# Kernel optimization log

Measured on AMD Instinct MI355X. Metric: run time of the kernel, lower is better.

The kernel has to match this reference:

```python
import jax, jax.numpy as jnp
import numpy as np

B, CIN, COUT, H, W = 8, 128, 256, 64, 64
EPS = 1e-5


def conv2d(x, w, b, pad):
    y = jax.lax.conv_general_dilated(
        x, w, window_strides=(1, 1), padding=[(pad, pad), (pad, pad)],
        dimension_numbers=('NCHW', 'OIHW', 'NCHW'))
    return y + b[None, :, None, None]


def deform_sample(x, offset):
    # x: [B,C,H,W], offset: [B,18,H,W] -> sampled: [B,C,9,H,W]
    b, c, h, w = x.shape
    off = offset.reshape(b, 9, 2, h, w)  # (dy, dx) per kernel tap (torchvision v1 order)
    ky = (jnp.arange(9) // 3 - 1).astype(x.dtype)
    kx = (jnp.arange(9) % 3 - 1).astype(x.dtype)
    py = jnp.arange(h, dtype=x.dtype)[None, None, :, None] + ky[None, :, None, None] + off[:, :, 0]
    px = jnp.arange(w, dtype=x.dtype)[None, None, None, :] + kx[None, :, None, None] + off[:, :, 1]
    y0 = jnp.floor(py); x0 = jnp.floor(px)
    fy = py - y0;       fx = px - x0
    xf = x.reshape(b, c, h * w)

    def gather(iy, ix):
        valid = (iy >= 0) & (iy < h) & (ix >= 0) & (ix < w)
        iyc = jnp.clip(iy, 0, h - 1).astype(jnp.int32)
        ixc = jnp.clip(ix, 0, w - 1).astype(jnp.int32)
        idx = (iyc * w + ixc).reshape(b, -1)  # [B, 9*H*W]
        g = jax.vmap(lambda xb, ib: jnp.take(xb, ib, axis=1))(xf, idx)  # [B,C,9HW]
        return g.reshape(b, c, 9, h, w) * valid.astype(x.dtype)[:, None]

    samp = (gather(y0,     x0    ) * ((1 - fy) * (1 - fx))[:, None]
          + gather(y0,     x0 + 1) * ((1 - fy) * fx      )[:, None]
          + gather(y0 + 1, x0    ) * (fy * (1 - fx)      )[:, None]
          + gather(y0 + 1, x0 + 1) * (fy * fx            )[:, None])
    return samp


def setup_inputs():
    key = jax.random.key(0)
    ks = jax.random.split(key, 8)
    return {
        'x':     jax.random.normal(ks[0], (B, CIN, H, W), jnp.float32),
        'w_off': jax.random.normal(ks[1], (18, CIN, 3, 3), jnp.float32) * 0.01,
        'b_off': jnp.zeros((18,), jnp.float32),
        'w_def': jax.random.normal(ks[2], (COUT, CIN, 3, 3), jnp.float32) * 0.03,
        'b_def': jax.random.normal(ks[3], (COUT,), jnp.float32) * 0.01,
        'gamma': jnp.ones((COUT,), jnp.float32),
        'beta':  jnp.zeros((COUT,), jnp.float32),
        'w_sc':  jax.random.normal(ks[4], (COUT, CIN, 1, 1), jnp.float32) * 0.05,
        'b_sc':  jnp.zeros((COUT,), jnp.float32),
    }


def reference(x, w_off, b_off, w_def, b_def, gamma, beta, w_sc, b_sc):
    offset = conv2d(x, w_off, b_off, pad=1)                 # [B,18,H,W]
    samp = deform_sample(x, offset)                         # [B,C,9,H,W]
    out = jnp.einsum('bckhw,ock->bohw', samp, w_def.reshape(COUT, CIN, 9))
    out = out + b_def[None, :, None, None]
    # BatchNorm2d (training mode: batch statistics)
    mean = out.mean(axis=(0, 2, 3))
    var = out.var(axis=(0, 2, 3))
    out = (out - mean[None, :, None, None]) * jax.lax.rsqrt(var + EPS)[None, :, None, None]
    out = out * gamma[None, :, None, None] + beta[None, :, None, None]
    out = out + conv2d(x, w_sc, b_sc, pad=0)                # residual shortcut (1x1)
    return jax.nn.relu(out)
```

## Files before the change

### kernel.cpp

```cpp
#include <hip/hip_runtime.h>

typedef __attribute__((ext_vector_type(8))) short bf16x8;
typedef __attribute__((ext_vector_type(4))) float f32x4;

__device__ __forceinline__ float bf2f(unsigned short u) {
  return __uint_as_float(((unsigned int)u) << 16);
}
__device__ __forceinline__ unsigned short f2bf(float f) {
  unsigned int u = __float_as_uint(f);
  u += 0x7fffu + ((u >> 16) & 1u);
  return (unsigned short)(u >> 16);
}

constexpr size_t OFF_XPAD = 0;
constexpr size_t SZ_XPAD  = (size_t)8 * 66 * 66 * 128 * 2;
constexpr size_t OFF_WB   = OFF_XPAD + SZ_XPAD;
constexpr size_t SZ_WB    = (size_t)9 * 16 * 256 * 8 * 2;
constexpr size_t OFF_WS2  = OFF_WB + SZ_WB;
constexpr size_t SZ_WS2   = (size_t)16 * 256 * 8 * 2;
constexpr size_t OFF_WO   = OFF_WS2 + SZ_WS2;
constexpr size_t SZ_WO    = (size_t)9 * 16 * 32 * 8 * 2;
constexpr size_t OFF_YM   = OFF_WO + SZ_WO;
constexpr size_t SZ_YM    = (size_t)32768 * 256 * 2;
constexpr size_t OFF_PART = OFF_YM + SZ_YM;
constexpr size_t SZ_PART  = (size_t)512 * 256 * 2 * 4;
constexpr size_t OFF_STAT = OFF_PART + SZ_PART;

__global__ __launch_bounds__(256) void k_prep_x(const float* __restrict__ x,
                                                unsigned short* __restrict__ xp) {
  int blk = blockIdx.x;
  int b = blk >> 6, h = blk & 63;
  int t = threadIdx.x;
  __shared__ float tile[16][66];
  for (int cc = 0; cc < 8; ++cc) {
    int c0 = cc * 16;
    int wr = t & 63, cl = t >> 6;
#pragma unroll
    for (int i = 0; i < 4; ++i) {
      int c = c0 + cl * 4 + i;
      tile[cl * 4 + i][wr] = x[(((size_t)b * 128 + c) * 64 + h) * 64 + wr];
    }
    __syncthreads();
    int ww = t >> 2, cq = t & 3;
    ushort4 u4;
    u4.x = f2bf(tile[cq * 4 + 0][ww]);
    u4.y = f2bf(tile[cq * 4 + 1][ww]);
    u4.z = f2bf(tile[cq * 4 + 2][ww]);
    u4.w = f2bf(tile[cq * 4 + 3][ww]);
    *(ushort4*)(xp + ((size_t)(b * 66 + h + 1) * 66 + (ww + 1)) * 128 + c0 + cq * 4) = u4;
    __syncthreads();
  }
}

__global__ __launch_bounds__(256) void k_pack_w(const float* __restrict__ wdef,
                                                const float* __restrict__ wsc,
                                                const float* __restrict__ woff,
                                                unsigned short* __restrict__ wB,
                                                unsigned short* __restrict__ wS,
                                                unsigned short* __restrict__ wO) {
  int tid = blockIdx.x * 256 + threadIdx.x;
  if (tid < 294912) {
    int k8 = tid & 7, n = (tid >> 3) & 255, kb = (tid >> 11) & 15, tap = tid >> 15;
    int c = kb * 8 + k8;
    wB[tid] = f2bf(wdef[((size_t)n * 128 + c) * 9 + tap]);
  } else if (tid < 294912 + 32768) {
    int i = tid - 294912;
    int k8 = i & 7, n = (i >> 3) & 255, kb = i >> 11;
    wS[i] = f2bf(wsc[(size_t)n * 128 + kb * 8 + k8]);
  } else if (tid < 294912 + 32768 + 36864) {
    int i = tid - 327680;
    int k8 = i & 7, n = (i >> 3) & 31, kb = (i >> 8) & 15, tap = i >> 12;
    int c = kb * 8 + k8;
    wO[i] = f2bf(n < 18 ? woff[((size_t)n * 128 + c) * 9 + tap] : 0.f);
  }
}

__global__ __launch_bounds__(256) void k_main(const unsigned short* __restrict__ xp,
                                              const unsigned short* __restrict__ wB,
                                              const unsigned short* __restrict__ wO,
                                              const float* __restrict__ boff,
                                              const float* __restrict__ bdef,
                                              unsigned short* __restrict__ ymain,
                                              float* __restrict__ partials) {
  int blk = blockIdx.x;
  int b = blk >> 6, h = blk & 63;
  int t = threadIdx.x;
  int lane = t & 63, wid = t >> 6;
  int m = lane & 15, quad = lane >> 4;
  __shared__ __align__(16) unsigned short At[2][64 * 136];
  __shared__ float offsL[9][64][2];

  {
    f32x4 a0 = {0.f, 0.f, 0.f, 0.f}, a1 = {0.f, 0.f, 0.f, 0.f};
    int px = wid * 16 + m;
    const unsigned short* xbase = xp + ((size_t)(b * 66 + h) * 66 + px) * 128 + quad * 8;
    for (int tap = 0; tap < 9; ++tap) {
      const unsigned short* arow = xbase + ((tap / 3) * 66 + (tap % 3)) * 128;
#pragma unroll
      for (int kk = 0; kk < 4; ++kk) {
        bf16x8 a = *(const bf16x8*)(arow + kk * 32);
        const unsigned short* bb = wO + (size_t)(tap * 16 + kk * 4 + quad) * 256;
        bf16x8 b0 = *(const bf16x8*)(bb + m * 8);
        bf16x8 b1 = *(const bf16x8*)(bb + (16 + m) * 8);
        a0 = __builtin_amdgcn_mfma_f32_16x16x32_bf16(a, b0, a0, 0, 0, 0);
        a1 = __builtin_amdgcn_mfma_f32_16x16x32_bf16(a, b1, a1, 0, 0, 0);
      }
    }
#pragma unroll
    for (int r = 0; r < 4; ++r) {
      int pxs = wid * 16 + quad * 4 + r;
      offsL[m >> 1][pxs][m & 1] = a0[r] + boff[m];
      if (m < 2) offsL[8][pxs][m] = a1[r] + boff[16 + m];
    }
  }
  __syncthreads();

  f32x4 acc[4][4];
#pragma unroll
  for (int i = 0; i < 4; ++i)
#pragma unroll
    for (int j = 0; j < 4; ++j) acc[i][j] = (f32x4){0.f, 0.f, 0.f, 0.f};

  int px_s = t >> 2, sub = t & 3;
  const unsigned short* xb_base = xp + (size_t)b * 66 * 66 * 128;
  int nb = wid * 64;

  auto sample_prep = [&](int tap, float* wgt, const unsigned short** p) {
    float2 ov = *(const float2*)&offsL[tap][px_s][0];
    int ky = tap / 3 - 1, kx = tap % 3 - 1;
    float py = (float)(h + ky) + ov.x;
    float pxf = (float)(px_s + kx) + ov.y;
    float y0f = floorf(py), x0f = floorf(pxf);
    float fy = py - y0f, fx = pxf - x0f;
    int iy0 = (int)y0f, ix0 = (int)x0f;
#pragma unroll
    for (int j = 0; j < 4; ++j) {
      int iy = iy0 + (j >> 1), ix = ix0 + (j & 1);
      float wy = (j >> 1) ? fy : 1.f - fy;
      float wx = (j & 1) ? fx : 1.f - fx;
      bool valid = (iy >= 0) && (iy < 64) && (ix >= 0) && (ix < 64);
      int iyc = min(max(iy, 0), 63), ixc = min(max(ix, 0), 63);
      wgt[j] = valid ? wy * wx : 0.f;
      p[j] = xb_base + ((size_t)(iyc + 1) * 66 + (ixc + 1)) * 128 + sub * 8;
    }
  };
  auto load_g2 = [&](const unsigned short** p, int g0, bf16x8 (*v)[4]) {
#pragma unroll
    for (int gg = 0; gg < 2; ++gg)
#pragma unroll
      for (int j = 0; j < 4; ++j)
        v[gg][j] = *(const bf16x8*)(p[j] + (g0 + gg) * 32);
  };
  auto store_g2 = [&](unsigned short* dst, int g0, const float* wgt, bf16x8 (*v)[4]) {
#pragma unroll
    for (int gg = 0; gg < 2; ++gg) {
      bf16x8 o;
#pragma unroll
      for (int j = 0; j < 8; ++j) {
        float s = fmaf(wgt[0], bf2f((unsigned short)v[gg][0][j]),
                  fmaf(wgt[1], bf2f((unsigned short)v[gg][1][j]),
                  fmaf(wgt[2], bf2f((unsigned short)v[gg][2][j]),
                       wgt[3] * bf2f((unsigned short)v[gg][3][j]))));
        o[j] = (short)f2bf(s);
      }
      *(bf16x8*)(dst + (g0 + gg) * 32) = o;
    }
  };
  auto mfma_half = [&](const unsigned short* buf, int tap, int kk0) {
#pragma unroll
    for (int kk = kk0; kk < kk0 + 2; ++kk) {
      bf16x8 af[4];
#pragma unroll
      for (int ms = 0; ms < 4; ++ms)
        af[ms] = *(const bf16x8*)(buf + (ms * 16 + m) * 136 + kk * 32 + quad * 8);
#pragma unroll
      for (int ns = 0; ns < 4; ++ns) {
        bf16x8 bfr = *(const bf16x8*)(wB + ((size_t)(tap * 16 + kk * 4 + quad) * 256 + nb + ns * 16 + m) * 8);
#pragma unroll
        for (int ms = 0; ms < 4; ++ms)
          acc[ms][ns] = __builtin_amdgcn_mfma_f32_16x16x32_bf16(af[ms], bfr, acc[ms][ns], 0, 0, 0);
      }
    }
  };

  {
    float wgt[4]; const unsigned short* p[4]; bf16x8 v[2][4];
    sample_prep(0, wgt, p);
    unsigned short* dst = &At[0][px_s * 136 + sub * 8];
    load_g2(p, 0, v); store_g2(dst, 0, wgt, v);
    load_g2(p, 2, v); store_g2(dst, 2, wgt, v);
  }
#pragma unroll
  for (int tap = 0; tap < 9; ++tap) {
    __syncthreads();
    const unsigned short* cur = At[tap & 1];
    unsigned short* dst = &At[(tap + 1) & 1][px_s * 136 + sub * 8];
    if (tap < 8) {
      float wgt[4]; const unsigned short* p[4]; bf16x8 v[2][4];
      sample_prep(tap + 1, wgt, p);
      load_g2(p, 0, v);
      mfma_half(cur, tap, 0);
      store_g2(dst, 0, wgt, v);
      load_g2(p, 2, v);
      mfma_half(cur, tap, 2);
      store_g2(dst, 2, wgt, v);
    } else {
      mfma_half(cur, tap, 0);
      mfma_half(cur, tap, 2);
    }
  }

  __syncthreads();
  unsigned short* yb = &At[0][0];
#pragma unroll
  for (int ns = 0; ns < 4; ++ns) {
    int n = nb + ns * 16 + m;
    float bias = bdef[n];
    float s = 0.f, q = 0.f;
#pragma unroll
    for (int ms = 0; ms < 4; ++ms) {
#pragma unroll
      for (int r = 0; r < 4; ++r) {
        int px = ms * 16 + quad * 4 + r;
        float v = acc[ms][ns][r] + bias;
        yb[px * 264 + n] = f2bf(v);
        s += v;
        q += v * v;
      }
    }
    s += __shfl_xor(s, 16); s += __shfl_xor(s, 32);
    q += __shfl_xor(q, 16); q += __shfl_xor(q, 32);
    if (quad == 0) {
      partials[((size_t)blk * 256 + n) * 2 + 0] = s;
      partials[((size_t)blk * 256 + n) * 2 + 1] = q;
    }
  }
  __syncthreads();
  {
    unsigned short* grow = ymain + (size_t)(blk * 64 + px_s) * 256;
    const unsigned short* lrow = yb + px_s * 264;
#pragma unroll
    for (int k = 0; k < 8; ++k) {
      int n0 = k * 32 + sub * 8;
      *(bf16x8*)(grow + n0) = *(const bf16x8*)(lrow + n0);
    }
  }
}

__global__ __launch_bounds__(64) void k_stats(const float* __restrict__ partials,
                                              const float* __restrict__ gamma,
                                              const float* __restrict__ beta,
                                              float* __restrict__ stats) {
  int ch = blockIdx.x;
  int L = threadIdx.x;
  float s = 0.f, q = 0.f;
#pragma unroll
  for (int i = 0; i < 8; ++i) {
    int row = i * 64 + L;
    s += partials[((size_t)row * 256 + ch) * 2 + 0];
    q += partials[((size_t)row * 256 + ch) * 2 + 1];
  }
#pragma unroll
  for (int d = 1; d < 64; d <<= 1) { s += __shfl_xor(s, d); q += __shfl_xor(q, d); }
  if (L == 0) {
    float mean = s * (1.f / 32768.f);
    float var = q * (1.f / 32768.f) - mean * mean;
    float inv = rsqrtf(var + 1e-5f);
    float A = gamma[ch] * inv;
    stats[ch * 2 + 0] = A;
    stats[ch * 2 + 1] = beta[ch] - mean * A;
  }
}

__global__ __launch_bounds__(256) void k_final(const unsigned short* __restrict__ xp,
                                               const unsigned short* __restrict__ wS,
                                               const unsigned short* __restrict__ ymain,
                                               const float* __restrict__ stats,
                                               const float* __restrict__ bsc,
                                               float* __restrict__ out) {
  int blk = blockIdx.x;
  int b = blk >> 6, h = blk & 63;
  int t = threadIdx.x;
  int lane = t & 63, wid = t >> 6;
  int m = lane & 15, quad = lane >> 4;
  __shared__ float tr[128 * 67];
  f32x4 acc[4][4];
#pragma unroll
  for (int i = 0; i < 4; ++i)
#pragma unroll
    for (int j = 0; j < 4; ++j) acc[i][j] = (f32x4){0.f, 0.f, 0.f, 0.f};
  const unsigned short* xrow = xp + ((size_t)(b * 66 + h + 1) * 66 + 1) * 128;
  int nb = wid * 64;
#pragma unroll
  for (int kk = 0; kk < 4; ++kk) {
    bf16x8 af[4];
#pragma unroll
    for (int ms = 0; ms < 4; ++ms)
      af[ms] = *(const bf16x8*)(xrow + (ms * 16 + m) * 128 + kk * 32 + quad * 8);
#pragma unroll
    for (int ns = 0; ns < 4; ++ns) {
      bf16x8 bfr = *(const bf16x8*)(wS + ((size_t)(kk * 4 + quad) * 256 + nb + ns * 16 + m) * 8);
#pragma unroll
      for (int ms = 0; ms < 4; ++ms)
        acc[ms][ns] = __builtin_amdgcn_mfma_f32_16x16x32_bf16(af[ms], bfr, acc[ms][ns], 0, 0, 0);
    }
  }
  for (int pass = 0; pass < 2; ++pass) {
    if ((wid >> 1) == pass) {
#pragma unroll
      for (int ns = 0; ns < 4; ++ns) {
        int n = nb + ns * 16 + m;
        float bs = bsc[n];
        int nl = n - pass * 128;
#pragma unroll
        for (int ms = 0; ms < 4; ++ms)
#pragma unroll
          for (int r = 0; r < 4; ++r) {
            int px = ms * 16 + quad * 4 + r;
            tr[nl * 67 + px] = acc[ms][ns][r] + bs;
          }
      }
    }
    __syncthreads();
    {
      int nl = t & 127, g = t >> 7;
      int n = pass * 128 + nl;
      float A = stats[n * 2], Bc = stats[n * 2 + 1];
#pragma unroll 8
      for (int i = 0; i < 32; ++i) {
        int px = g * 32 + i;
        float ym = bf2f(ymain[(size_t)(blk * 64 + px) * 256 + n]);
        float* pt = &tr[nl * 67 + px];
        *pt = fmaxf(fmaf(ym, A, Bc) + *pt, 0.f);
      }
    }
    __syncthreads();
    {
      int ww = t & 63, ng = t >> 6;
#pragma unroll 8
      for (int i = 0; i < 32; ++i) {
        int nl = ng * 32 + i;
        out[((size_t)(b * 256 + pass * 128 + nl) * 64 + h) * 64 + ww] = tr[nl * 67 + ww];
      }
    }
    __syncthreads();
  }
}

extern "C" void kernel_launch(void* const* d_in, const int* in_sizes, int n_in,
                              void* d_out, int out_size, void* d_ws, size_t ws_size,
                              hipStream_t stream) {
  const float* x     = (const float*)d_in[0];
  const float* w_off = (const float*)d_in[1];
  const float* b_off = (const float*)d_in[2];
  const float* w_def = (const float*)d_in[3];
  const float* b_def = (const float*)d_in[4];
  const float* gamma = (const float*)d_in[5];
  const float* beta  = (const float*)d_in[6];
  const float* w_sc  = (const float*)d_in[7];
  const float* b_sc  = (const float*)d_in[8];
  float* out = (float*)d_out;

  char* ws = (char*)d_ws;
  unsigned short* xpad  = (unsigned short*)(ws + OFF_XPAD);
  unsigned short* wB    = (unsigned short*)(ws + OFF_WB);
  unsigned short* wS    = (unsigned short*)(ws + OFF_WS2);
  unsigned short* wO    = (unsigned short*)(ws + OFF_WO);
  unsigned short* ymain = (unsigned short*)(ws + OFF_YM);
  float* partials       = (float*)(ws + OFF_PART);
  float* stats          = (float*)(ws + OFF_STAT);

  hipMemsetAsync(xpad, 0, SZ_XPAD, stream);
  k_prep_x<<<512, 256, 0, stream>>>(x, xpad);
  k_pack_w<<<1424, 256, 0, stream>>>(w_def, w_sc, w_off, wB, wS, wO);
  k_main<<<512, 256, 0, stream>>>(xpad, wB, wO, b_off, b_def, ymain, partials);
  k_stats<<<256, 64, 0, stream>>>(partials, gamma, beta, stats);
  k_final<<<512, 256, 0, stream>>>(xpad, wS, ymain, stats, b_sc, out);
}
```

Before: 162.1 us.

## Fuse main, stats and final into one persistent kernel with grid barriers

Merges the deformable conv, the BatchNorm statistics reduction and the residual/ReLU epilogue into one kernel that keeps accumulators in registers across two software grid barriers. This removes the bf16 ymain round-trip to global memory and two kernel launches. Blocks grow to 512 threads with warp specialisation: producer waves sample the next tap while consumer waves run MFMA, and the producers also compute the 1x1 shortcut. The full memset of the padded input becomes a border-only zero fill, and the x-prep and weight-pack kernels are merged into one. The grid barrier requires all 512 blocks to be co-resident, which risks deadlock if occupancy is insufficient, and the heavy LDS use may lower occupancy.

New measurement: 245.7 us. 51.5% more time.

```diff
diff --git a/kernel.cpp b/kernel.cpp
--- a/kernel.cpp
+++ b/kernel.cpp
@@ -1,4 +1,5 @@
 #include <hip/hip_runtime.h>
+#include <hip/hip_bf16.h>
 
 typedef __attribute__((ext_vector_type(8))) short bf16x8;
 typedef __attribute__((ext_vector_type(4))) float f32x4;
@@ -20,79 +21,122 @@
 constexpr size_t SZ_WS2   = (size_t)16 * 256 * 8 * 2;
 constexpr size_t OFF_WO   = OFF_WS2 + SZ_WS2;
 constexpr size_t SZ_WO    = (size_t)9 * 16 * 32 * 8 * 2;
-constexpr size_t OFF_YM   = OFF_WO + SZ_WO;
-constexpr size_t SZ_YM    = (size_t)32768 * 256 * 2;
-constexpr size_t OFF_PART = OFF_YM + SZ_YM;
+constexpr size_t OFF_PART = OFF_WO + SZ_WO;
 constexpr size_t SZ_PART  = (size_t)512 * 256 * 2 * 4;
 constexpr size_t OFF_STAT = OFF_PART + SZ_PART;
-
-__global__ __launch_bounds__(256) void k_prep_x(const float* __restrict__ x,
-                                                unsigned short* __restrict__ xp) {
+constexpr size_t SZ_STAT  = (size_t)256 * 2 * 4;
+constexpr size_t OFF_CNT  = OFF_STAT + SZ_STAT;
+constexpr size_t SZ_CNT   = 2 * 4;
+
+__device__ __forceinline__ void grid_barrier(unsigned int* cnt, unsigned int target) {
+  __syncthreads();
+  if (threadIdx.x == 0) {
+    __threadfence();
+    __hip_atomic_fetch_add(cnt, 1u, __ATOMIC_ACQ_REL, __HIP_MEMORY_SCOPE_AGENT);
+    while (__hip_atomic_load(cnt, __ATOMIC_ACQUIRE, __HIP_MEMORY_SCOPE_AGENT) < target) {
+      __builtin_amdgcn_s_sleep(16);
+    }
+  }
+  __syncthreads();
+}
+
+__global__ __launch_bounds__(256) void k_prep(const float* __restrict__ x,
+                                              const float* __restrict__ wdef,
+                                              const float* __restrict__ wsc,
+                                              const float* __restrict__ woff,
+                                              unsigned short* __restrict__ xp,
+                                              unsigned short* __restrict__ wB,
+                                              unsigned short* __restrict__ wS,
+                                              unsigned short* __restrict__ wO) {
   int blk = blockIdx.x;
-  int b = blk >> 6, h = blk & 63;
   int t = threadIdx.x;
-  __shared__ float tile[16][66];
-  for (int cc = 0; cc < 8; ++cc) {
-    int c0 = cc * 16;
-    int wr = t & 63, cl = t >> 6;
-#pragma unroll
-    for (int i = 0; i < 4; ++i) {
-      int c = c0 + cl * 4 + i;
-      tile[cl * 4 + i][wr] = x[(((size_t)b * 128 + c) * 64 + h) * 64 + wr];
-    }
-    __syncthreads();
-    int ww = t >> 2, cq = t & 3;
-    ushort4 u4;
-    u4.x = f2bf(tile[cq * 4 + 0][ww]);
-    u4.y = f2bf(tile[cq * 4 + 1][ww]);
-    u4.z = f2bf(tile[cq * 4 + 2][ww]);
-    u4.w = f2bf(tile[cq * 4 + 3][ww]);
-    *(ushort4*)(xp + ((size_t)(b * 66 + h + 1) * 66 + (ww + 1)) * 128 + c0 + cq * 4) = u4;
-    __syncthreads();
-  }
-}
-
-__global__ __launch_bounds__(256) void k_pack_w(const float* __restrict__ wdef,
-                                                const float* __restrict__ wsc,
-                                                const float* __restrict__ woff,
-                                                unsigned short* __restrict__ wB,
-                                                unsigned short* __restrict__ wS,
-                                                unsigned short* __restrict__ wO) {
-  int tid = blockIdx.x * 256 + threadIdx.x;
-  if (tid < 294912) {
-    int k8 = tid & 7, n = (tid >> 3) & 255, kb = (tid >> 11) & 15, tap = tid >> 15;
-    int c = kb * 8 + k8;
-    wB[tid] = f2bf(wdef[((size_t)n * 128 + c) * 9 + tap]);
-  } else if (tid < 294912 + 32768) {
-    int i = tid - 294912;
-    int k8 = i & 7, n = (i >> 3) & 255, kb = i >> 11;
-    wS[i] = f2bf(wsc[(size_t)n * 128 + kb * 8 + k8]);
-  } else if (tid < 294912 + 32768 + 36864) {
-    int i = tid - 327680;
-    int k8 = i & 7, n = (i >> 3) & 31, kb = (i >> 8) & 15, tap = i >> 12;
-    int c = kb * 8 + k8;
-    wO[i] = f2bf(n < 18 ? woff[((size_t)n * 128 + c) * 9 + tap] : 0.f);
-  }
-}
-
-__global__ __launch_bounds__(256) void k_main(const unsigned short* __restrict__ xp,
-                                              const unsigned short* __restrict__ wB,
-                                              const unsigned short* __restrict__ wO,
-                                              const float* __restrict__ boff,
-                                              const float* __restrict__ bdef,
-                                              unsigned short* __restrict__ ymain,
-                                              float* __restrict__ partials) {
-  int blk = blockIdx.x;
-  int b = blk >> 6, h = blk & 63;
+  if (blk < 1024) {
+    int b = blk >> 7, h = (blk >> 1) & 63, chalf = blk & 1;
+    __shared__ float tile[16][66];
+    for (int cc = 0; cc < 4; ++cc) {
+      int c0 = (chalf * 4 + cc) * 16;
+      int wr = t & 63, cl = t >> 6;
+#pragma unroll
+      for (int i = 0; i < 4; ++i) {
+        int c = c0 + cl * 4 + i;
+        tile[cl * 4 + i][wr] = x[(((size_t)b * 128 + c) * 64 + h) * 64 + wr];
+      }
+      __syncthreads();
+      int ww = t >> 2, cq = t & 3;
+      ushort4 u4;
+      u4.x = f2bf(tile[cq * 4 + 0][ww]);
+      u4.y = f2bf(tile[cq * 4 + 1][ww]);
+      u4.z = f2bf(tile[cq * 4 + 2][ww]);
+      u4.w = f2bf(tile[cq * 4 + 3][ww]);
+      *(ushort4*)(xp + ((size_t)(b * 66 + h + 1) * 66 + (ww + 1)) * 128 + c0 + cq * 4) = u4;
+      __syncthreads();
+    }
+  } else if (blk < 1040) {
+    int idx = blk - 1024;
+    int b = idx >> 1, hp = (idx & 1) ? 65 : 0;
+    unsigned short* base = xp + (size_t)(b * 66 + hp) * 66 * 128;
+    uint4 z = {0u, 0u, 0u, 0u};
+#pragma unroll
+    for (int it = 0; it < 5; ++it) {
+      int i = it * 256 + t;
+      if (i < 1056) *(uint4*)(base + i * 8) = z;
+    }
+  } else if (blk < 1056) {
+    int idx = blk - 1040;
+    int b = idx >> 1, px = (idx & 1) ? 65 : 0;
+    uint4 z = {0u, 0u, 0u, 0u};
+#pragma unroll
+    for (int it = 0; it < 4; ++it) {
+      int row = it * 16 + (t >> 4);
+      int off = t & 15;
+      *(uint4*)(xp + ((size_t)(b * 66 + 1 + row) * 66 + px) * 128 + off * 8) = z;
+    }
+  } else {
+    int tid = (blk - 1056) * 256 + t;
+    if (tid < 294912) {
+      int k8 = tid & 7, n = (tid >> 3) & 255, kb = (tid >> 11) & 15, tap = tid >> 15;
+      int c = kb * 8 + k8;
+      wB[tid] = f2bf(wdef[((size_t)n * 128 + c) * 9 + tap]);
+    } else if (tid < 294912 + 32768) {
+      int i = tid - 294912;
+      int k8 = i & 7, n = (i >> 3) & 255, kb = i >> 11;
+      wS[i] = f2bf(wsc[(size_t)n * 128 + kb * 8 + k8]);
+    } else if (tid < 294912 + 32768 + 36864) {
+      int i = tid - 327680;
+      int k8 = i & 7, n = (i >> 3) & 31, kb = (i >> 8) & 15, tap = i >> 12;
+      int c = kb * 8 + k8;
+      wO[i] = f2bf(n < 18 ? woff[((size_t)n * 128 + c) * 9 + tap] : 0.f);
+    }
+  }
+}
+
+__global__ __launch_bounds__(512, 4) void k_coop(const unsigned short* __restrict__ xp,
+                                                 const unsigned short* __restrict__ wB,
+                                                 const unsigned short* __restrict__ wS,
+                                                 const unsigned short* __restrict__ wO,
+                                                 const float* __restrict__ boff,
+                                                 const float* __restrict__ bdef,
+                                                 const float* __restrict__ gamma,
+                                                 const float* __restrict__ beta,
+                                                 const float* __restrict__ bsc,
+                                                 float* __restrict__ partials,
+                                                 float* __restrict__ stats,
+                                                 unsigned int* __restrict__ cnt,
+                                                 float* __restrict__ out) {
+  int rt = blockIdx.x;
+  int b = rt >> 6, h = rt & 63;
   int t = threadIdx.x;
   int lane = t & 63, wid = t >> 6;
   int m = lane & 15, quad = lane >> 4;
+  bool consumer = wid < 4;
   __shared__ __align__(16) unsigned short At[2][64 * 136];
+  __shared__ __align__(16) unsigned short sb[256 * 68];
   __shared__ float offsL[9][64][2];
 
-  {
+  if (!consumer) {
+    int pw = wid - 4;
     f32x4 a0 = {0.f, 0.f, 0.f, 0.f}, a1 = {0.f, 0.f, 0.f, 0.f};
-    int px = wid * 16 + m;
+    int px = pw * 16 + m;
     const unsigned short* xbase = xp + ((size_t)(b * 66 + h) * 66 + px) * 128 + quad * 8;
     for (int tap = 0; tap < 9; ++tap) {
       const unsigned short* arow = xbase + ((tap / 3) * 66 + (tap % 3)) * 128;
@@ -108,22 +152,16 @@
     }
 #pragma unroll
     for (int r = 0; r < 4; ++r) {
-      int pxs = wid * 16 + quad * 4 + r;
+      int pxs = pw * 16 + quad * 4 + r;
       offsL[m >> 1][pxs][m & 1] = a0[r] + boff[m];
       if (m < 2) offsL[8][pxs][m] = a1[r] + boff[16 + m];
     }
   }
   __syncthreads();
 
-  f32x4 acc[4][4];
-#pragma unroll
-  for (int i = 0; i < 4; ++i)
-#pragma unroll
-    for (int j = 0; j < 4; ++j) acc[i][j] = (f32x4){0.f, 0.f, 0.f, 0.f};
-
-  int px_s = t >> 2, sub = t & 3;
+  int pl = t & 255;
+  int px_s = pl >> 2, sub = pl & 3;
   const unsigned short* xb_base = xp + (size_t)b * 66 * 66 * 128;
-  int nb = wid * 64;
 
   auto sample_prep = [&](int tap, float* wgt, const unsigned short** p) {
     float2 ov = *(const float2*)&offsL[tap][px_s][0];
@@ -144,206 +182,183 @@
       p[j] = xb_base + ((size_t)(iyc + 1) * 66 + (ixc + 1)) * 128 + sub * 8;
     }
   };
-  auto load_g2 = [&](const unsigned short** p, int g0, bf16x8 (*v)[4]) {
-#pragma unroll
-    for (int gg = 0; gg < 2; ++gg)
-#pragma unroll
-      for (int j = 0; j < 4; ++j)
-        v[gg][j] = *(const bf16x8*)(p[j] + (g0 + gg) * 32);
+  auto sample_tap = [&](int tap, unsigned short* dst) {
+    float wgt[4]; const unsigned short* p[4];
+    sample_prep(tap, wgt, p);
+#pragma unroll
+    for (int g0 = 0; g0 < 4; g0 += 2) {
+      bf16x8 v[2][4];
+#pragma unroll
+      for (int gg = 0; gg < 2; ++gg)
+#pragma unroll
+        for (int j = 0; j < 4; ++j)
+          v[gg][j] = *(const bf16x8*)(p[j] + (g0 + gg) * 32);
+#pragma unroll
+      for (int gg = 0; gg < 2; ++gg) {
+        bf16x8 o;
+#pragma unroll
+        for (int j = 0; j < 8; ++j) {
+          float s = fmaf(wgt[0], bf2f((unsigned short)v[gg][0][j]),
+                    fmaf(wgt[1], bf2f((unsigned short)v[gg][1][j]),
+                    fmaf(wgt[2], bf2f((unsigned short)v[gg][2][j]),
+                         wgt[3] * bf2f((unsigned short)v[gg][3][j]))));
+          o[j] = (short)f2bf(s);
+        }
+        *(bf16x8*)(dst + (g0 + gg) * 32) = o;
+      }
+    }
   };
-  auto store_g2 = [&](unsigned short* dst, int g0, const float* wgt, bf16x8 (*v)[4]) {
-#pragma unroll
-    for (int gg = 0; gg < 2; ++gg) {
-      bf16x8 o;
-#pragma unroll
-      for (int j = 0; j < 8; ++j) {
-        float s = fmaf(wgt[0], bf2f((unsigned short)v[gg][0][j]),
-                  fmaf(wgt[1], bf2f((unsigned short)v[gg][1][j]),
-                  fmaf(wgt[2], bf2f((unsigned short)v[gg][2][j]),
-                       wgt[3] * bf2f((unsigned short)v[gg][3][j]))));
-        o[j] = (short)f2bf(s);
-      }
-      *(bf16x8*)(dst + (g0 + gg) * 32) = o;
-    }
-  };
-  auto mfma_half = [&](const unsigned short* buf, int tap, int kk0) {
-#pragma unroll
-    for (int kk = kk0; kk < kk0 + 2; ++kk) {
-      bf16x8 af[4];
+
+  f32x4 acc[4][4];
+  if (consumer) {
+#pragma unroll
+    for (int i = 0; i < 4; ++i)
+#pragma unroll
+      for (int j = 0; j < 4; ++j) acc[i][j] = (f32x4){0.f, 0.f, 0.f, 0.f};
+  }
+  int nb = wid * 64;
+
+  if (!consumer) sample_tap(0, &At[0][px_s * 136 + sub * 8]);
+  __syncthreads();
+
+#pragma unroll
+  for (int tap = 0; tap < 9; ++tap) {
+    if (consumer) {
+      const unsigned short* cur = At[tap & 1];
+#pragma unroll
+      for (int kk = 0; kk < 4; ++kk) {
+        bf16x8 af[4];
+#pragma unroll
+        for (int ms = 0; ms < 4; ++ms)
+          af[ms] = *(const bf16x8*)(cur + (ms * 16 + m) * 136 + kk * 32 + quad * 8);
+#pragma unroll
+        for (int ns = 0; ns < 4; ++ns) {
+          bf16x8 bfr = *(const bf16x8*)(wB + ((size_t)(tap * 16 + kk * 4 + quad) * 256 + nb + ns * 16 + m) * 8);
+#pragma unroll
+          for (int ms = 0; ms < 4; ++ms)
+            acc[ms][ns] = __builtin_amdgcn_mfma_f32_16x16x32_bf16(af[ms], bfr, acc[ms][ns], 0, 0, 0);
+        }
+      }
+    } else if (tap < 8) {
+      sample_tap(tap + 1, &At[(tap + 1) & 1][px_s * 136 + sub * 8]);
+    }
+    __syncthreads();
+  }
+
+  if (consumer) {
+#pragma unroll
+    for (int ns = 0; ns < 4; ++ns) {
+      int n = nb + ns * 16 + m;
+      float bias = bdef[n];
+      float s = 0.f, q = 0.f;
 #pragma unroll
       for (int ms = 0; ms < 4; ++ms)
-        af[ms] = *(const bf16x8*)(buf + (ms * 16 + m) * 136 + kk * 32 + quad * 8);
+#pragma unroll
+        for (int r = 0; r < 4; ++r) {
+          float v = acc[ms][ns][r] + bias;
+          s += v; q += v * v;
+        }
+      s += __shfl_xor(s, 16); s += __shfl_xor(s, 32);
+      q += __shfl_xor(q, 16); q += __shfl_xor(q, 32);
+      if (quad == 0) {
+        partials[((size_t)rt * 256 + n) * 2 + 0] = s;
+        partials[((size_t)rt * 256 + n) * 2 + 1] = q;
+      }
+    }
+  }
+
+  grid_barrier(cnt + 0, 512);
+
+  if (rt < 256) {
+    int ch = rt;
+    int row = wid * 64 + lane;
+    float s = partials[((size_t)row * 256 + ch) * 2 + 0];
+    float q = partials[((size_t)row * 256 + ch) * 2 + 1];
+#pragma unroll
+    for (int d = 1; d < 64; d <<= 1) { s += __shfl_xor(s, d); q += __shfl_xor(q, d); }
+    float* red = &offsL[0][0][0];
+    if (lane == 0) { red[wid * 2] = s; red[wid * 2 + 1] = q; }
+    __syncthreads();
+    if (wid == 0 && lane < 8) {
+      s = red[lane * 2]; q = red[lane * 2 + 1];
+#pragma unroll
+      for (int d = 1; d < 8; d <<= 1) { s += __shfl_xor(s, d); q += __shfl_xor(q, d); }
+      if (lane == 0) {
+        float mean = s * (1.f / 32768.f);
+        float var = q * (1.f / 32768.f) - mean * mean;
+        float A = gamma[ch] * rsqrtf(var + 1e-5f);
+        stats[ch * 2 + 0] = A;
+        stats[ch * 2 + 1] = beta[ch] - mean * A;
+      }
+    }
+  }
+
+  grid_barrier(cnt + 1, 512);
+
+  unsigned short* yb = &At[0][0];
+  if (consumer) {
+#pragma unroll
+    for (int ns = 0; ns < 4; ++ns) {
+      int n = nb + ns * 16 + m;
+      float bias = bdef[n];
+      float A = stats[n * 2], Bc = stats[n * 2 + 1];
+#pragma unroll
+      for (int ms = 0; ms < 4; ++ms) {
+        ushort4 u;
+        u.x = f2bf(fmaf(acc[ms][ns][0] + bias, A, Bc));
+        u.y = f2bf(fmaf(acc[ms][ns][1] + bias, A, Bc));
+        u.z = f2bf(fmaf(acc[ms][ns][2] + bias, A, Bc));
+        u.w = f2bf(fmaf(acc[ms][ns][3] + bias, A, Bc));
+        *(ushort4*)(yb + n * 68 + ms * 16 + quad * 4) = u;
+      }
+    }
+  }
+  if (!consumer) {
+    int nbp = (wid - 4) * 64;
+    const unsigned short* xrow = xp + ((size_t)(b * 66 + h + 1) * 66 + 1) * 128;
+    f32x4 acc2[4][4];
+#pragma unroll
+    for (int i = 0; i < 4; ++i)
+#pragma unroll
+      for (int j = 0; j < 4; ++j) acc2[i][j] = (f32x4){0.f, 0.f, 0.f, 0.f};
+#pragma unroll
+    for (int kk = 0; kk < 4; ++kk) {
+      bf16x8 xf[4];
+#pragma unroll
+      for (int ms = 0; ms < 4; ++ms)
+        xf[ms] = *(const bf16x8*)(xrow + (ms * 16 + m) * 128 + kk * 32 + quad * 8);
 #pragma unroll
       for (int ns = 0; ns < 4; ++ns) {
-        bf16x8 bfr = *(const bf16x8*)(wB + ((size_t)(tap * 16 + kk * 4 + quad) * 256 + nb + ns * 16 + m) * 8);
+        bf16x8 wf = *(const bf16x8*)(wS + ((size_t)(kk * 4 + quad) * 256 + nbp + ns * 16 + m) * 8);
 #pragma unroll
         for (int ms = 0; ms < 4; ++ms)
-          acc[ms][ns] = __builtin_amdgcn_mfma_f32_16x16x32_bf16(af[ms], bfr, acc[ms][ns], 0, 0, 0);
-      }
-    }
-  };
-
+          acc2[ms][ns] = __builtin_amdgcn_mfma_f32_16x16x32_bf16(xf[ms], wf, acc2[ms][ns], 0, 0, 0);
+      }
+    }
+#pragma unroll
+    for (int ns = 0; ns < 4; ++ns) {
+      int n = nbp + ns * 16 + m;
+      float bsv = bsc[n];
+#pragma unroll
+      for (int ms = 0; ms < 4; ++ms) {
+        ushort4 u;
+        u.x = f2bf(acc2[ms][ns][0] + bsv);
+        u.y = f2bf(acc2[ms][ns][1] + bsv);
+        u.z = f2bf(acc2[ms][ns][2] + bsv);
+        u.w = f2bf(acc2[ms][ns][3] + bsv);
+        *(ushort4*)(sb + n * 68 + ms * 16 + quad * 4) = u;
+      }
+    }
+  }
+  __syncthreads();
   {
-    float wgt[4]; const unsigned short* p[4]; bf16x8 v[2][4];
-    sample_prep(0, wgt, p);
-    unsigned short* dst = &At[0][px_s * 136 + sub * 8];
-    load_g2(p, 0, v); store_g2(dst, 0, wgt, v);
-    load_g2(p, 2, v); store_g2(dst, 2, wgt, v);
-  }
-#pragma unroll
-  for (int tap = 0; tap < 9; ++tap) {
-    __syncthreads();
-    const unsigned short* cur = At[tap & 1];
-    unsigned short* dst = &At[(tap + 1) & 1][px_s * 136 + sub * 8];
-    if (tap < 8) {
-      float wgt[4]; const unsigned short* p[4]; bf16x8 v[2][4];
-      sample_prep(tap + 1, wgt, p);
-      load_g2(p, 0, v);
-      mfma_half(cur, tap, 0);
-      store_g2(dst, 0, wgt, v);
-      load_g2(p, 2, v);
-      mfma_half(cur, tap, 2);
-      store_g2(dst, 2, wgt, v);
-    } else {
-      mfma_half(cur, tap, 0);
-      mfma_half(cur, tap, 2);
-    }
-  }
-
-  __syncthreads();
-  unsigned short* yb = &At[0][0];
-#pragma unroll
-  for (int ns = 0; ns < 4; ++ns) {
-    int n = nb + ns * 16 + m;
-    float bias = bdef[n];
-    float s = 0.f, q = 0.f;
-#pragma unroll
-    for (int ms = 0; ms < 4; ++ms) {
-#pragma unroll
-      for (int r = 0; r < 4; ++r) {
-        int px = ms * 16 + quad * 4 + r;
-        float v = acc[ms][ns][r] + bias;
-        yb[px * 264 + n] = f2bf(v);
-        s += v;
-        q += v * v;
-      }
-    }
-    s += __shfl_xor(s, 16); s += __shfl_xor(s, 32);
-    q += __shfl_xor(q, 16); q += __shfl_xor(q, 32);
-    if (quad == 0) {
-      partials[((size_t)blk * 256 + n) * 2 + 0] = s;
-      partials[((size_t)blk * 256 + n) * 2 + 1] = q;
-    }
-  }
-  __syncthreads();
-  {
-    unsigned short* grow = ymain + (size_t)(blk * 64 + px_s) * 256;
-    const unsigned short* lrow = yb + px_s * 264;
-#pragma unroll
-    for (int k = 0; k < 8; ++k) {
-      int n0 = k * 32 + sub * 8;
-      *(bf16x8*)(grow + n0) = *(const bf16x8*)(lrow + n0);
-    }
-  }
-}
-
-__global__ __launch_bounds__(64) void k_stats(const float* __restrict__ partials,
-                                              const float* __restrict__ gamma,
-                                              const float* __restrict__ beta,
-                                              float* __restrict__ stats) {
-  int ch = blockIdx.x;
-  int L = threadIdx.x;
-  float s = 0.f, q = 0.f;
-#pragma unroll
-  for (int i = 0; i < 8; ++i) {
-    int row = i * 64 + L;
-    s += partials[((size_t)row * 256 + ch) * 2 + 0];
-    q += partials[((size_t)row * 256 + ch) * 2 + 1];
-  }
-#pragma unroll
-  for (int d = 1; d < 64; d <<= 1) { s += __shfl_xor(s, d); q += __shfl_xor(q, d); }
-  if (L == 0) {
-    float mean = s * (1.f / 32768.f);
-    float var = q * (1.f / 32768.f) - mean * mean;
-    float inv = rsqrtf(var + 1e-5f);
-    float A = gamma[ch] * inv;
-    stats[ch * 2 + 0] = A;
-    stats[ch * 2 + 1] = beta[ch] - mean * A;
-  }
-}
-
-__global__ __launch_bounds__(256) void k_final(const unsigned short* __restrict__ xp,
-                                               const unsigned short* __restrict__ wS,
-                                               const unsigned short* __restrict__ ymain,
-                                               const float* __restrict__ stats,
-                                               const float* __restrict__ bsc,
-                                               float* __restrict__ out) {
-  int blk = blockIdx.x;
-  int b = blk >> 6, h = blk & 63;
-  int t = threadIdx.x;
-  int lane = t & 63, wid = t >> 6;
-  int m = lane & 15, quad = lane >> 4;
-  __shared__ float tr[128 * 67];
-  f32x4 acc[4][4];
-#pragma unroll
-  for (int i = 0; i < 4; ++i)
-#pragma unroll
-    for (int j = 0; j < 4; ++j) acc[i][j] = (f32x4){0.f, 0.f, 0.f, 0.f};
-  const unsigned short* xrow = xp + ((size_t)(b * 66 + h + 1) * 66 + 1) * 128;
-  int nb = wid * 64;
-#pragma unroll
-  for (int kk = 0; kk < 4; ++kk) {
-    bf16x8 af[4];
-#pragma unroll
-    for (int ms = 0; ms < 4; ++ms)
-      af[ms] = *(const bf16x8*)(xrow + (ms * 16 + m) * 128 + kk * 32 + quad * 8);
-#pragma unroll
-    for (int ns = 0; ns < 4; ++ns) {
-      bf16x8 bfr = *(const bf16x8*)(wS + ((size_t)(kk * 4 + quad) * 256 + nb + ns * 16 + m) * 8);
-#pragma unroll
-      for (int ms = 0; ms < 4; ++ms)
-        acc[ms][ns] = __builtin_amdgcn_mfma_f32_16x16x32_bf16(af[ms], bfr, acc[ms][ns], 0, 0, 0);
-    }
-  }
-  for (int pass = 0; pass < 2; ++pass) {
-    if ((wid >> 1) == pass) {
-#pragma unroll
-      for (int ns = 0; ns < 4; ++ns) {
-        int n = nb + ns * 16 + m;
-        float bs = bsc[n];
-        int nl = n - pass * 128;
-#pragma unroll
-        for (int ms = 0; ms < 4; ++ms)
-#pragma unroll
-          for (int r = 0; r < 4; ++r) {
-            int px = ms * 16 + quad * 4 + r;
-            tr[nl * 67 + px] = acc[ms][ns][r] + bs;
-          }
-      }
-    }
-    __syncthreads();
-    {
-      int nl = t & 127, g = t >> 7;
-      int n = pass * 128 + nl;
-      float A = stats[n * 2], Bc = stats[n * 2 + 1];
+    int px = t & 63, chg = t >> 6;
 #pragma unroll 8
-      for (int i = 0; i < 32; ++i) {
-        int px = g * 32 + i;
-        float ym = bf2f(ymain[(size_t)(blk * 64 + px) * 256 + n]);
-        float* pt = &tr[nl * 67 + px];
-        *pt = fmaxf(fmaf(ym, A, Bc) + *pt, 0.f);
-      }
-    }
-    __syncthreads();
-    {
-      int ww = t & 63, ng = t >> 6;
-#pragma unroll 8
-      for (int i = 0; i < 32; ++i) {
-        int nl = ng * 32 + i;
-        out[((size_t)(b * 256 + pass * 128 + nl) * 64 + h) * 64 + ww] = tr[nl * 67 + ww];
-      }
-    }
-    __syncthreads();
+    for (int i = 0; i < 32; ++i) {
+      int ch = chg * 32 + i;
+      float v = bf2f(yb[ch * 68 + px]) + bf2f(sb[ch * 68 + px]);
+      out[(((size_t)(b * 256 + ch) * 64 + h) * 64) + px] = fmaxf(v, 0.f);
+    }
   }
 }
 
@@ -366,14 +381,12 @@
   unsigned short* wB    = (unsigned short*)(ws + OFF_WB);
   unsigned short* wS    = (unsigned short*)(ws + OFF_WS2);
   unsigned short* wO    = (unsigned short*)(ws + OFF_WO);
-  unsigned short* ymain = (unsigned short*)(ws + OFF_YM);
   float* partials       = (float*)(ws + OFF_PART);
   float* stats          = (float*)(ws + OFF_STAT);
-
-  hipMemsetAsync(xpad, 0, SZ_XPAD, stream);
-  k_prep_x<<<512, 256, 0, stream>>>(x, xpad);
-  k_pack_w<<<1424, 256, 0, stream>>>(w_def, w_sc, w_off, wB, wS, wO);
-  k_main<<<512, 256, 0, stream>>>(xpad, wB, wO, b_off, b_def, ymain, partials);
-  k_stats<<<256, 64, 0, stream>>>(partials, gamma, beta, stats);
-  k_final<<<512, 256, 0, stream>>>(xpad, wS, ymain, stats, b_sc, out);
-}
+  unsigned int* cnt     = (unsigned int*)(ws + OFF_CNT);
+
+  hipMemsetAsync(cnt, 0, SZ_CNT, stream);
+  k_prep<<<2480, 256, 0, stream>>>(x, w_def, w_sc, w_off, xpad, wB, wS, wO);
+  k_coop<<<512, 512, 0, stream>>>(xpad, wB, wS, wO, b_off, b_def, gamma, beta, b_sc,
+                                  partials, stats, cnt, out);
+}
```
